# Optimization experiments

Measured on AMD Instinct MI355X. Metric: run time of the kernel, lower is better.

The kernel has to match this reference:

```python
import jax, jax.numpy as jnp
import numpy as np

SHAPES = ((64, 64), (32, 32), (16, 16))   # H/8, H/16, H/32 levels of a 512x512 image
B, D = 32, 256
NH, L, P = 8, 3, 4                        # MSDeformAttn heads / levels / points
DH = D // NH
NCLS, NC, NH_CA = 200, 10, 2
LQ = 32 * 32
LIN = sum(h * w for h, w in SHAPES)


def _ref_points():
    # get_reference_points for the H/16 grid, normalized (x, y) in (0,1)
    H_, W_ = 32, 32
    ry, rx = np.meshgrid(np.linspace(0.5, H_ - 0.5, H_) / H_,
                         np.linspace(0.5, W_ - 0.5, W_) / W_, indexing='ij')
    ref = np.stack([rx.ravel(), ry.ravel()], -1).astype(np.float32)  # (Lq, 2)
    return jnp.asarray(ref)[None, :, None, :]                        # (1, Lq, 1, 2)


def _msda(query, feats, W_off, b_off, W_attn, b_attn, W_val, b_val, W_out, b_out):
    """Multi-scale deformable attention (grid_sample bilinear, align_corners=False, zero pad)."""
    value = (feats @ W_val + b_val).reshape(B, LIN, NH, DH)
    off = (query @ W_off + b_off).reshape(B, LQ, NH, L, P, 2)
    aw = jax.nn.softmax((query @ W_attn + b_attn).reshape(B, LQ, NH, L * P), -1)
    aw = aw.reshape(B, LQ, NH, L, P)
    norm = jnp.asarray([[w, h] for h, w in SHAPES], jnp.float32)     # (L, 2) as (W, H)
    ref = _ref_points()                                              # (1, Lq, 1, 2)
    loc = ref[:, :, None, :, None, :] + off / norm[None, None, None, :, None, :]  # (B,Lq,NH,L,P,2)

    out = jnp.zeros((B, NH, LQ, DH), query.dtype)
    start = 0
    for lvl, (H_, W_) in enumerate(SHAPES):
        v = value[:, start:start + H_ * W_].transpose(0, 2, 1, 3)    # (B, NH, HW, DH)
        start += H_ * W_
        lx = loc[:, :, :, lvl, :, 0] * W_ - 0.5                      # (B, Lq, NH, P)
        ly = loc[:, :, :, lvl, :, 1] * H_ - 0.5
        x0 = jnp.floor(lx).astype(jnp.int32)
        y0 = jnp.floor(ly).astype(jnp.int32)
        dx = (lx - x0).transpose(0, 2, 1, 3)                         # (B, NH, Lq, P)
        dy = (ly - y0).transpose(0, 2, 1, 3)

        def gather(ix, iy):
            valid = (ix >= 0) & (ix < W_) & (iy >= 0) & (iy < H_)
            idx = (jnp.clip(iy, 0, H_ - 1) * W_ + jnp.clip(ix, 0, W_ - 1))
            idx = idx.transpose(0, 2, 1, 3).reshape(B, NH, LQ * P)
            g = jnp.take_along_axis(v, idx[..., None], axis=2).reshape(B, NH, LQ, P, DH)
            return g * valid.transpose(0, 2, 1, 3)[..., None]

        samp = (gather(x0,     y0)     * ((1 - dx) * (1 - dy))[..., None]
              + gather(x0 + 1, y0)     * (dx * (1 - dy))[..., None]
              + gather(x0,     y0 + 1) * ((1 - dx) * dy)[..., None]
              + gather(x0 + 1, y0 + 1) * (dx * dy)[..., None])       # (B,NH,Lq,P,DH)
        out = out + (samp * aw[:, :, :, lvl, :].transpose(0, 2, 1, 3)[..., None]).sum(3)
    out = out.transpose(0, 2, 1, 3).reshape(B, LQ, D)
    return out @ W_out + b_out


def _cross_attn(x, concepts, Wq, bq, Wkv, bkv, Wp, bp):
    Bx, N, _ = x.shape
    M = concepts.shape[1]
    dh = D // NH_CA
    q = (x @ Wq + bq).reshape(Bx, N, NH_CA, dh).transpose(0, 2, 1, 3)          # (B, h, N, dh)
    kv = (concepts @ Wkv + bkv).reshape(1, M, 2, NH_CA, dh).transpose(2, 0, 3, 1, 4)
    k, v = kv[0], kv[1]                                                        # (1, h, M, dh)
    attn = jax.nn.softmax(jnp.einsum('bhnd,ohmd->bhnm', q, k) * (dh ** -0.5), -1)
    o = jnp.einsum('bhnm,ohmd->bhnd', attn, v).transpose(0, 2, 1, 3).reshape(Bx, N, D)
    return o @ Wp + bp, attn


def _forward(query, feats, x_cls, W_off, b_off, W_attn, b_attn, W_val, b_val, W_out, b_out,
             unsup_concepts, concepts, spatial_concepts,
             Wq_c, bq_c, Wkv_c, bkv_c, Wp_c, bp_c,
             Wq_s, bq_s, Wkv_s, bkv_s, Wp_s, bp_s):
    # injector-style residual: query tokens refined by multi-scale deformable attention
    x = query + _msda(query, feats, W_off, b_off, W_attn, b_attn, W_val, b_val, W_out, b_out)
    # NB: original code reuses concept_tranformer for the unsup branch (faithful to source)
    out_u, attn_u = _cross_attn(x_cls, unsup_concepts, Wq_c, bq_c, Wkv_c, bkv_c, Wp_c, bp_c)
    out_n, attn_n = _cross_attn(x_cls, concepts,       Wq_c, bq_c, Wkv_c, bkv_c, Wp_c, bp_c)
    out_s, attn_s = _cross_attn(x,     spatial_concepts, Wq_s, bq_s, Wkv_s, bkv_s, Wp_s, bp_s)
    out = out_u[:, 0] + out_n[:, 0] + out_s.mean(1)                  # (B, num_classes)
    return out, attn_u.mean(1), attn_n.mean(1), attn_s.mean(1)


def setup_inputs() -> dict:
    key = jax.random.key(0)
    ks = jax.random.split(key, 20)
    s = 1.0 / np.sqrt(D)

    def n(i, shape, scale=1.0):
        return jax.random.normal(ks[i], shape, jnp.float32) * scale

    return dict(
        query=n(0, (B, LQ, D)), feats=n(1, (B, LIN, D)), x_cls=n(2, (B, 1, D)),
        W_off=n(3, (D, NH * L * P * 2), 0.01), b_off=n(4, (NH * L * P * 2,), 0.5),
        W_attn=n(5, (D, NH * L * P), 0.01), b_attn=jnp.zeros((NH * L * P,)),
        W_val=n(6, (D, D), s), b_val=jnp.zeros((D,)),
        W_out=n(7, (D, D), s), b_out=jnp.zeros((D,)),
        unsup_concepts=n(8, (1, NC, D), s), concepts=n(9, (1, NC, D), s),
        spatial_concepts=n(10, (1, NC, D), s),
        Wq_c=n(11, (D, D), s), bq_c=jnp.zeros((D,)),
        Wkv_c=n(12, (D, 2 * D), s), bkv_c=jnp.zeros((2 * D,)),
        Wp_c=n(13, (D, NCLS), s), bp_c=jnp.zeros((NCLS,)),
        Wq_s=n(14, (D, D), s), bq_s=jnp.zeros((D,)),
        Wkv_s=n(15, (D, 2 * D), s), bkv_s=jnp.zeros((2 * D,)),
        Wp_s=n(16, (D, NCLS), s), bp_s=jnp.zeros((NCLS,)),
    )


def reference(query, feats, x_cls, W_off, b_off, W_attn, b_attn, W_val, b_val, W_out, b_out,
              unsup_concepts, concepts, spatial_concepts,
              Wq_c, bq_c, Wkv_c, bkv_c, Wp_c, bp_c,
              Wq_s, bq_s, Wkv_s, bkv_s, Wp_s, bp_s):
    return _forward(query, feats, x_cls, W_off, b_off, W_attn, b_attn, W_val, b_val, W_out, b_out,
                    unsup_concepts, concepts, spatial_concepts,
                    Wq_c, bq_c, Wkv_c, bkv_c, Wp_c, bp_c,
                    Wq_s, bq_s, Wkv_s, bkv_s, Wp_s, bp_s)
```

## Files before the change

kernel.cpp:

```cpp
#include <hip/hip_runtime.h>
#include <hip/hip_bf16.h>


typedef __attribute__((ext_vector_type(8))) short s16x8;
typedef __attribute__((ext_vector_type(4))) float f32x4;

__device__ __forceinline__ void store_val(float* p, float v) { *p = v; }
__device__ __forceinline__ void store_val(__hip_bfloat16* p, float v) { *p = __float2bfloat16(v); }

__device__ __forceinline__ unsigned short f2bf(float x) {
  unsigned int u = __builtin_bit_cast(unsigned int, x);
  u += 0x7FFFu + ((u >> 16) & 1u);
  return (unsigned short)(u >> 16);
}
__device__ __forceinline__ float bf2f(unsigned short u) {
  return __builtin_bit_cast(float, (unsigned int)u << 16);
}
__device__ __forceinline__ float bflo(unsigned int u) {
  return __builtin_bit_cast(float, u << 16);
}
__device__ __forceinline__ float bfhi(unsigned int u) {
  return __builtin_bit_cast(float, u & 0xFFFF0000u);
}

__device__ __forceinline__ void gload16(const char* g, char* l) {
  __builtin_amdgcn_global_load_lds(
      (const __attribute__((address_space(1))) unsigned int*)g,
      (__attribute__((address_space(3))) unsigned int*)l, 16, 0, 0);
}

__global__ __launch_bounds__(256) void prep_all(
    const float* __restrict__ W_val, const float* __restrict__ W_off,
    const float* __restrict__ b_off, const float* __restrict__ W_attn,
    const float* __restrict__ b_attn, char* __restrict__ imgV,
    char* __restrict__ imgQ, float* __restrict__ bpack,
    const float* __restrict__ unsup, const float* __restrict__ conc,
    const float* __restrict__ spat, const float* __restrict__ Wkv_c,
    const float* __restrict__ bkv_c, const float* __restrict__ Wkv_s,
    const float* __restrict__ bkv_s, float* __restrict__ kv_u,
    float* __restrict__ kv_n, float* __restrict__ kv_s,
    const float* __restrict__ Wq_s, const float* __restrict__ bq_s,
    const float* __restrict__ W_out, const float* __restrict__ b_out,
    float* __restrict__ WLt, float* __restrict__ WL2t, float* __restrict__ cL)
{
  const int bi = blockIdx.x;
  const int tid = threadIdx.x;
  if (bi <= 576) {
    const int n = bi, k = tid;
    if (n == 576) {
      bpack[k] = (k < 192) ? b_off[k] : ((k < 288) ? b_attn[k - 192] : 0.f);
      if (k < 64) bpack[256 + k] = (k < 32) ? b_attn[64 + k] : 0.f;
      return;
    }
    const int ks = k >> 6;
    const int kb = (k & 63) * 2;
    if (n < 256) {
      const unsigned short v = f2bf(W_val[(size_t)k * 256 + n]);
      *(unsigned short*)(imgV + ks * 32768 + n * 128 + (kb ^ ((n & 7) << 4))) = v;
    } else {
      const int c = n - 256;
      float v = 0.f;
      if (c < 192) v = W_off[(size_t)k * 192 + c];
      else if (c < 288) v = W_attn[(size_t)k * 96 + (c - 192)];
      *(unsigned short*)(imgQ + ks * 40960 + c * 128 + (kb ^ ((c & 7) << 4))) = f2bf(v);
    }
    return;
  }
  if (bi <= 579) {
    const int j = bi - 577;
    const float* src = (j == 0) ? unsup : ((j == 1) ? conc : spat);
    const float* W   = (j < 2) ? Wkv_c : Wkv_s;
    const float* bb  = (j < 2) ? bkv_c : bkv_s;
    float* dst       = (j == 0) ? kv_u : ((j == 1) ? kv_n : kv_s);
    __shared__ float s[2560];
    for (int i = tid; i < 2560; i += 256) s[i] = src[i];
    __syncthreads();
    for (int o = tid; o < 5120; o += 256) {
      const int m = o >> 9, n = o & 511;
      float acc = bb[n];
      for (int k = 0; k < 256; ++k) acc += s[m * 256 + k] * W[(size_t)k * 512 + n];
      dst[o] = acc;
    }
    return;
  }
  {
    const int j = bi - 580;
    const int h = j / 10, m = j % 10;
    __shared__ float kk[128], wl[256], bred[256];
    if (tid < 128) {
      const int n = h * 128 + tid;
      float acc = bkv_s[n];
      for (int k = 0; k < 256; ++k) acc += spat[m * 256 + k] * Wkv_s[(size_t)k * 512 + n];
      kk[tid] = acc;
    }
    __syncthreads();
    float acc = 0.f;
    for (int e = 0; e < 128; ++e) acc += Wq_s[(size_t)tid * 256 + h * 128 + e] * kk[e];
    wl[tid] = acc;
    __syncthreads();
    float acc2 = 0.f;
    for (int t = 0; t < 256; ++t) acc2 += W_out[(size_t)tid * 256 + t] * wl[t];
    const float scale = 0.08838834764831845f;
    WLt[j * 256 + tid] = scale * acc;
    WL2t[j * 256 + tid] = scale * acc2;
    bred[tid] = b_out[tid] * wl[tid] + ((tid < 128) ? bq_s[h * 128 + tid] * kk[tid] : 0.f);
    __syncthreads();
    for (int s = 128; s > 0; s >>= 1) {
      if (tid < s) bred[tid] += bred[tid + s];
      __syncthreads();
    }
    if (tid == 0) cL[j] = scale * bred[0];
  }
}

template <typename OT, int NCOLS, int MINW, bool HM>
__global__ __launch_bounds__(512, MINW) void gemm_f32a(
    const float* __restrict__ A, const char* __restrict__ Bimg,
    const float* __restrict__ bias, OT* __restrict__ C)
{
  constexpr int NFR = NCOLS / 64;
  __shared__ char sAf[32768];
  __shared__ char sBb[NCOLS * 128];

  const int tid = threadIdx.x;
  const int lane = tid & 63;
  const int w = tid >> 6;
  const int wr = (w >> 2) * 64;
  const int wc = (w & 3) * (NCOLS / 4);
  const int l15 = lane & 15;
  const int lg = lane >> 4;
  const int m0 = blockIdx.x * 128;

  int asrc[4];
#pragma unroll
  for (int i = 0; i < 4; ++i) {
    const int slot = w * 256 + i * 64 + lane;
    const int row = slot >> 4;
    const int c = (slot & 15) ^ (row & 7);
    asrc[i] = row * 256 + c * 4;
  }
  const float* Abase = A + (size_t)m0 * 256;

  f32x4 acc[4][NFR] = {};

#pragma unroll
  for (int ks = 0; ks < 4; ++ks) {
    if (ks) __syncthreads();
    {
      char* la = sAf + w * 4096;
#pragma unroll
      for (int i = 0; i < 4; ++i)
        gload16((const char*)(Abase + ks * 64 + asrc[i]), la + i * 1024);
      const char* gb = Bimg + ks * (NCOLS * 128) + w * (NCOLS * 16) + lane * 16;
      char* lb = sBb + w * (NCOLS * 16);
#pragma unroll
      for (int i = 0; i < NFR; ++i)
        gload16(gb + i * 1024, lb + i * 1024);
    }
    __syncthreads();
#pragma unroll
    for (int kk = 0; kk < 2; ++kk) {
      const int c0 = kk * 8 + lg * 2;
      s16x8 af[4];
#pragma unroll
      for (int mf = 0; mf < 4; ++mf) {
        const int row = wr + mf * 16 + l15;
        const int sw = row & 7;
        const f32x4 lo = *reinterpret_cast<const f32x4*>(
            sAf + row * 256 + ((c0 ^ sw) * 16));
        const f32x4 hi = *reinterpret_cast<const f32x4*>(
            sAf + row * 256 + (((c0 + 1) ^ sw) * 16));
        uint4 u;
        u.x = (unsigned)f2bf(lo[0]) | ((unsigned)f2bf(lo[1]) << 16);
        u.y = (unsigned)f2bf(lo[2]) | ((unsigned)f2bf(lo[3]) << 16);
        u.z = (unsigned)f2bf(hi[0]) | ((unsigned)f2bf(hi[1]) << 16);
        u.w = (unsigned)f2bf(hi[2]) | ((unsigned)f2bf(hi[3]) << 16);
        af[mf] = __builtin_bit_cast(s16x8, u);
      }
      const int kb = kk * 64 + lg * 16;
      s16x8 bf[NFR];
#pragma unroll
      for (int nf = 0; nf < NFR; ++nf) {
        const int col = wc + nf * 16 + l15;
        bf[nf] = *reinterpret_cast<const s16x8*>(sBb + col * 128 + (kb ^ ((col & 7) << 4)));
      }
#pragma unroll
      for (int mf = 0; mf < 4; ++mf)
#pragma unroll
        for (int nf = 0; nf < NFR; ++nf)
          acc[mf][nf] = __builtin_amdgcn_mfma_f32_16x16x32_bf16(af[mf], bf[nf], acc[mf][nf], 0, 0, 0);
    }
  }

#pragma unroll
  for (int nf = 0; nf < NFR; ++nf) {
    const int col = wc + nf * 16 + l15;
    const float bb = bias[col];
#pragma unroll
    for (int mf = 0; mf < 4; ++mf) {
#pragma unroll
      for (int j = 0; j < 4; ++j) {
        const int row = m0 + wr + mf * 16 + lg * 4 + j;
        const float v = acc[mf][nf][j] + bb;
        if constexpr (HM) {
          const unsigned rb = (unsigned)row / 5376u;
          const unsigned rr = (unsigned)row - rb * 5376u;
          store_val(&C[(((size_t)rb * 8 + (col >> 5)) * 5376 + rr) * 32 + (col & 31)], v);
        } else {
          store_val(&C[(size_t)row * NCOLS + col], v);
        }
      }
    }
  }
}

__global__ __launch_bounds__(256) void msda_v4(
    const float* __restrict__ offlog, const __hip_bfloat16* __restrict__ value,
    __hip_bfloat16* __restrict__ msda_out)
{
  const int bq0 = blockIdx.x * 8;
  const int b = bq0 >> 10;
  const int tid = threadIdx.x;
  __shared__ float aw[768];
  __shared__ int4 sRow[768];
  __shared__ float4 sW[768];
  __shared__ __align__(16) char gbuf[4 * 3 * 4096];

  if (tid < 64) {
    const int qi = tid >> 3, h = tid & 7;
    const float* lp = &offlog[(size_t)(bq0 + qi) * 320 + 192 + h * 12];
    float e[12];
    float mx = -1e30f;
#pragma unroll
    for (int i = 0; i < 12; ++i) { e[i] = lp[i]; mx = fmaxf(mx, e[i]); }
    float s = 0.f;
#pragma unroll
    for (int i = 0; i < 12; ++i) { e[i] = expf(e[i] - mx); s += e[i]; }
    const float inv = 1.f / s;
#pragma unroll
    for (int i = 0; i < 12; ++i) aw[qi * 96 + h * 12 + i] = e[i] * inv;
  }
  __syncthreads();

#pragma unroll
  for (int k = 0; k < 3; ++k) {
    const int j = k * 256 + tid;
    const int qi = j / 96, cc = j - qi * 96;
    const int q = (bq0 + qi) & 1023;
    const int h = cc / 12, r = cc - h * 12, l = r >> 2, p_ = r & 3;
    const int WHl[3] = {64, 32, 16};
    const int St[3] = {0, 4096, 5120};
    const float2 o2 = *reinterpret_cast<const float2*>(
        &offlog[(size_t)(bq0 + qi) * 320 + h * 24 + l * 8 + p_ * 2]);
    const float refx = ((q & 31) + 0.5f) * (1.0f / 32.0f);
    const float refy = ((q >> 5) + 0.5f) * (1.0f / 32.0f);
    const int WH = WHl[l];
    const float fw = (float)WH;
    const float lx = (refx + o2.x / fw) * fw - 0.5f;
    const float ly = (refy + o2.y / fw) * fw - 0.5f;
    const float fx = floorf(lx), fy = floorf(ly);
    const int x0 = (int)fx, y0 = (int)fy;
    const float dx = lx - fx, dy = ly - fy;
    const float a = aw[j];
    int rows[4];
    float ws[4];
#pragma unroll
    for (int c = 0; c < 4; ++c) {
      const int ix = x0 + (c & 1), iy = y0 + (c >> 1);
      const float wb = ((c & 1) ? dx : 1.f - dx) * ((c >> 1) ? dy : 1.f - dy);
      const bool valid = (ix >= 0) && (ix < WH) && (iy >= 0) && (iy < WH);
      const int cx = min(max(ix, 0), WH - 1);
      const int cy = min(max(iy, 0), WH - 1);
      rows[c] = St[l] + cy * WH + cx;
      ws[c] = valid ? wb * a : 0.f;
    }
    sRow[j] = int4{rows[0], rows[1], rows[2], rows[3]};
    sW[j] = float4{ws[0], ws[1], ws[2], ws[3]};
  }
  __syncthreads();

  const int w = tid >> 6;
  const int lane = tid & 63;
  const int qi = tid >> 5;
  const int h = (tid >> 2) & 7;
  const int d4 = tid & 3;
  const unsigned short* vb = (const unsigned short*)value
      + ((size_t)b * 8 + h) * 5376 * 32 + d4 * 8;
  const int cbase = qi * 96 + h * 12;
  char* gb = gbuf + w * 12288;

#pragma unroll
  for (int s0 = 0; s0 < 2; ++s0) {
    const int4 rows = sRow[cbase + s0];
    const int ra[4] = {rows.x, rows.y, rows.z, rows.w};
#pragma unroll
    for (int c = 0; c < 4; ++c)
      gload16((const char*)(vb + (size_t)ra[c] * 32), gb + s0 * 4096 + c * 1024);
  }

  float acc[8] = {};
#pragma unroll
  for (int s = 0; s < 12; ++s) {
    if (s + 2 < 12) {
      const int4 rows = sRow[cbase + s + 2];
      const int ra[4] = {rows.x, rows.y, rows.z, rows.w};
      const int slot = (s + 2) % 3;
#pragma unroll
      for (int c = 0; c < 4; ++c)
        gload16((const char*)(vb + (size_t)ra[c] * 32), gb + slot * 4096 + c * 1024);
    }
    if (s <= 9)       asm volatile("s_waitcnt vmcnt(8)" ::: "memory");
    else if (s == 10) asm volatile("s_waitcnt vmcnt(4)" ::: "memory");
    else              asm volatile("s_waitcnt vmcnt(0)" ::: "memory");
    __builtin_amdgcn_sched_barrier(0);
    const float4 wv = sW[cbase + s];
    const float wa[4] = {wv.x, wv.y, wv.z, wv.w};
    const int slot = s % 3;
#pragma unroll
    for (int c = 0; c < 4; ++c) {
      const uint4 v = *reinterpret_cast<const uint4*>(gb + slot * 4096 + c * 1024 + lane * 16);
      const float wgt = wa[c];
      acc[0] += wgt * bflo(v.x); acc[1] += wgt * bfhi(v.x);
      acc[2] += wgt * bflo(v.y); acc[3] += wgt * bfhi(v.y);
      acc[4] += wgt * bflo(v.z); acc[5] += wgt * bfhi(v.z);
      acc[6] += wgt * bflo(v.w); acc[7] += wgt * bfhi(v.w);
    }
  }
  uint4 o;
  o.x = (unsigned)f2bf(acc[0]) | ((unsigned)f2bf(acc[1]) << 16);
  o.y = (unsigned)f2bf(acc[2]) | ((unsigned)f2bf(acc[3]) << 16);
  o.z = (unsigned)f2bf(acc[4]) | ((unsigned)f2bf(acc[5]) << 16);
  o.w = (unsigned)f2bf(acc[6]) | ((unsigned)f2bf(acc[7]) << 16);
  *reinterpret_cast<uint4*>(
      (unsigned short*)msda_out + (size_t)(bq0 + qi) * 256 + h * 32 + d4 * 8) = o;
}

__global__ __launch_bounds__(256) void spatial_kernel(
    const float* __restrict__ query, const __hip_bfloat16* __restrict__ msda,
    const float* __restrict__ WLt, const float* __restrict__ WL2t,
    const float* __restrict__ cL, float* __restrict__ attn_out,
    float* __restrict__ partial)
{
  __shared__ float wls[20][256];
  __shared__ float wl2s[20][256];
  __shared__ float red[128][20];
  const int tid = threadIdx.x;
  for (int i = tid; i < 5120; i += 256) {
    wls[i >> 8][i & 255] = WLt[i];
    wl2s[i >> 8][i & 255] = WL2t[i];
  }
  const int row_local = tid >> 1;
  const int half = tid & 1;
  const int row = blockIdx.x * 128 + row_local;
  float acc[20];
#pragma unroll
  for (int c = 0; c < 20; ++c) acc[c] = half ? 0.f : cL[c];
  __syncthreads();

  const float* qp = &query[(size_t)row * 256 + half * 128];
  const unsigned short* mp = (const unsigned short*)msda + (size_t)row * 256 + half * 128;
  const int kbase = half * 128;
  for (int k = 0; k < 128; k += 4) {
    const f32x4 q4 = *reinterpret_cast<const f32x4*>(qp + k);
    const uint2 mm = *reinterpret_cast<const uint2*>(mp + k);
    const float m0 = bf2f((unsigned short)mm.x);
    const float m1 = bf2f((unsigned short)(mm.x >> 16));
    const float m2 = bf2f((unsigned short)mm.y);
    const float m3 = bf2f((unsigned short)(mm.y >> 16));
#pragma unroll
    for (int c = 0; c < 20; ++c) {
      const f32x4 w4 = *reinterpret_cast<const f32x4*>(&wls[c][kbase + k]);
      const f32x4 v4 = *reinterpret_cast<const f32x4*>(&wl2s[c][kbase + k]);
      acc[c] += q4.x * w4.x + q4.y * w4.y + q4.z * w4.z + q4.w * w4.w
              + m0 * v4.x + m1 * v4.y + m2 * v4.z + m3 * v4.w;
    }
  }
  if (half == 1) {
#pragma unroll
    for (int c = 0; c < 20; ++c) red[row_local][c] = acc[c];
  }
  __syncthreads();
  if (half == 0) {
    float a[20];
#pragma unroll
    for (int c = 0; c < 20; ++c) a[c] = acc[c] + red[row_local][c];
#pragma unroll
    for (int h = 0; h < 2; ++h) {
      float mx = -1e30f;
#pragma unroll
      for (int m = 0; m < 10; ++m) mx = fmaxf(mx, a[h * 10 + m]);
      float s = 0.f;
#pragma unroll
      for (int m = 0; m < 10; ++m) { a[h * 10 + m] = expf(a[h * 10 + m] - mx); s += a[h * 10 + m]; }
      const float inv = 1.f / s;
#pragma unroll
      for (int m = 0; m < 10; ++m) a[h * 10 + m] *= inv;
    }
#pragma unroll
    for (int m = 0; m < 10; ++m)
      attn_out[(size_t)row * 10 + m] = 0.5f * (a[m] + a[10 + m]);
#pragma unroll
    for (int c = 0; c < 20; ++c) red[row_local][c] = a[c];
  }
  __syncthreads();
  if (tid < 20) {
    float s = 0.f;
    for (int r = 0; r < 128; ++r) s += red[r][tid];
    partial[blockIdx.x * 20 + tid] = s;
  }
}

__global__ __launch_bounds__(256) void final2_kernel(
    const float* __restrict__ x_cls, const float* __restrict__ Wq_c,
    const float* __restrict__ bq_c, const float* __restrict__ kv_u,
    const float* __restrict__ kv_n, const float* __restrict__ partial,
    const float* __restrict__ kv_s, const float* __restrict__ Wp_c,
    const float* __restrict__ bp_c, const float* __restrict__ Wp_s,
    const float* __restrict__ bp_s, float* __restrict__ out,
    float* __restrict__ attn_u_out, float* __restrict__ attn_n_out)
{
  const int b = blockIdx.x, tid = threadIdx.x;
  __shared__ float ou[256], osb[256], abar[20], xr[256];
  if (tid < 64)
    *reinterpret_cast<float4*>(&xr[tid * 4]) =
        *reinterpret_cast<const float4*>(&x_cls[(size_t)b * 256 + tid * 4]);
  if (tid >= 64 && tid < 84) {
    const int c = tid - 64;
    float s = 0.f;
    for (int ch = 0; ch < 8; ++ch) s += partial[(b * 8 + ch) * 20 + c];
    abar[c] = s * (1.0f / 1024.0f);
  }
  __syncthreads();
  if (tid < 64) {
    const int lane = tid;
    float4 q4 = *reinterpret_cast<const float4*>(&bq_c[lane * 4]);
    for (int k = 0; k < 256; ++k) {
      const float xk = xr[k];
      const float4 w = *reinterpret_cast<const float4*>(&Wq_c[(size_t)k * 256 + lane * 4]);
      q4.x += xk * w.x; q4.y += xk * w.y; q4.z += xk * w.z; q4.w += xk * w.w;
    }
    const float scale = 0.08838834764831845f;
    float4 osum = {0.f, 0.f, 0.f, 0.f};
    for (int cs = 0; cs < 2; ++cs) {
      const float* kv = cs ? kv_n : kv_u;
      float* aout = cs ? attn_n_out : attn_u_out;
      float attn[10];
      float mx = -1e30f;
#pragma unroll
      for (int m = 0; m < 10; ++m) {
        const float4 k4 = *reinterpret_cast<const float4*>(&kv[m * 512 + lane * 4]);
        float p = q4.x * k4.x + q4.y * k4.y + q4.z * k4.z + q4.w * k4.w;
        p += __shfl_xor(p, 1);  p += __shfl_xor(p, 2);  p += __shfl_xor(p, 4);
        p += __shfl_xor(p, 8);  p += __shfl_xor(p, 16);
        attn[m] = p * scale;
        mx = fmaxf(mx, attn[m]);
      }
      float s = 0.f;
#pragma unroll
      for (int m = 0; m < 10; ++m) { attn[m] = expf(attn[m] - mx); s += attn[m]; }
      const float inv = 1.f / s;
#pragma unroll
      for (int m = 0; m < 10; ++m) {
        attn[m] *= inv;
        const float am = 0.5f * (attn[m] + __shfl_xor(attn[m], 32));
        if (lane == m) aout[b * 10 + m] = am;
        const float4 v4 = *reinterpret_cast<const float4*>(&kv[m * 512 + 256 + lane * 4]);
        osum.x += attn[m] * v4.x; osum.y += attn[m] * v4.y;
        osum.z += attn[m] * v4.z; osum.w += attn[m] * v4.w;
      }
    }
    *reinterpret_cast<float4*>(&ou[lane * 4]) = osum;
  }
  {
    const int h = tid >> 7, d = tid & 127;
    float s = 0.f;
#pragma unroll
    for (int m = 0; m < 10; ++m) s += abar[h * 10 + m] * kv_s[m * 512 + 256 + h * 128 + d];
    osb[tid] = s;
  }
  __syncthreads();
  if (tid < 200) {
    float acc = 2.f * bp_c[tid] + bp_s[tid];
    for (int dd = 0; dd < 256; ++dd)
      acc += ou[dd] * Wp_c[dd * 200 + tid] + osb[dd] * Wp_s[dd * 200 + tid];
    out[b * 200 + tid] = acc;
  }
}

extern "C" void kernel_launch(void* const* d_in, const int* in_sizes, int n_in,
                              void* d_out, int out_size, void* d_ws, size_t ws_size,
                              hipStream_t stream)
{
  const float* query  = (const float*)d_in[0];
  const float* feats  = (const float*)d_in[1];
  const float* x_cls  = (const float*)d_in[2];
  const float* W_off  = (const float*)d_in[3];
  const float* b_off  = (const float*)d_in[4];
  const float* W_attn = (const float*)d_in[5];
  const float* b_attn = (const float*)d_in[6];
  const float* W_val  = (const float*)d_in[7];
  const float* b_val  = (const float*)d_in[8];
  const float* W_out  = (const float*)d_in[9];
  const float* b_out  = (const float*)d_in[10];
  const float* unsup  = (const float*)d_in[11];
  const float* conc   = (const float*)d_in[12];
  const float* spat   = (const float*)d_in[13];
  const float* Wq_c   = (const float*)d_in[14];
  const float* bq_c   = (const float*)d_in[15];
  const float* Wkv_c  = (const float*)d_in[16];
  const float* bkv_c  = (const float*)d_in[17];
  const float* Wp_c   = (const float*)d_in[18];
  const float* bp_c   = (const float*)d_in[19];
  const float* Wq_s   = (const float*)d_in[20];
  const float* bq_s   = (const float*)d_in[21];
  const float* Wkv_s  = (const float*)d_in[22];
  const float* bkv_s  = (const float*)d_in[23];
  const float* Wp_s   = (const float*)d_in[24];
  const float* bp_s   = (const float*)d_in[25];
  float* out = (float*)d_out;

  const int B = 32, LQ = 1024, LIN = 5376;
  const int MQ = B * LQ;
  const int MV = B * LIN;

  char* p = (char*)d_ws;
  __hip_bfloat16* value = (__hip_bfloat16*)p;   p += (size_t)MV * 256 * 2;
  float* offlog   = (float*)p;                  p += (size_t)MQ * 320 * 4;
  __hip_bfloat16* msda = (__hip_bfloat16*)p;    p += (size_t)MQ * 256 * 2;
  char* imgV      = p;                          p += 4 * 32768;
  char* imgQ      = p;                          p += 4 * 40960;
  float* bpack    = (float*)p;                  p += 320 * 4;
  float* kv_u     = (float*)p;                  p += 5120 * 4;
  float* kv_n     = (float*)p;                  p += 5120 * 4;
  float* kv_s     = (float*)p;                  p += 5120 * 4;
  float* WLt      = (float*)p;                  p += 5120 * 4;
  float* WL2t     = (float*)p;                  p += 5120 * 4;
  float* cL       = (float*)p;                  p += 32 * 4;
  float* partial  = (float*)p;                  p += 256 * 20 * 4;

  dim3 blk(256);
  prep_all<<<dim3(600), blk, 0, stream>>>(
      W_val, W_off, b_off, W_attn, b_attn, imgV, imgQ, bpack,
      unsup, conc, spat, Wkv_c, bkv_c, Wkv_s, bkv_s, kv_u, kv_n, kv_s,
      Wq_s, bq_s, W_out, b_out, WLt, WL2t, cL);
  gemm_f32a<__hip_bfloat16, 256, 4, true><<<dim3(MV / 128), dim3(512), 0, stream>>>(
      feats, imgV, b_val, value);
  gemm_f32a<float, 320, 2, false><<<dim3(MQ / 128), dim3(512), 0, stream>>>(
      query, imgQ, bpack, offlog);
  msda_v4<<<dim3(MQ / 8), blk, 0, stream>>>(offlog, value, msda);
  spatial_kernel<<<dim3(MQ / 128), blk, 0, stream>>>(
      query, msda, WLt, WL2t, cL, out + 7040, partial);
  final2_kernel<<<dim3(B), blk, 0, stream>>>(
      x_cls, Wq_c, bq_c, kv_u, kv_n, partial, kv_s, Wp_c, bp_c, Wp_s, bp_s,
      out, out + 6400, out + 6720);
}
```

Baseline: 317.5 us.

## Fuse spatial concept-attention logits into MSDA kernel epilogue

Merges the spatial_kernel into the deformable attention kernel: each thread dots its fp32 MSDA accumulator slice and query slice against the fused weight rows, then reduces across 32 lanes with shuffles before computing the softmax. This removes the bf16 MSDA intermediate buffer's write and read and one kernel launch. In exchange, every thread in the MSDA kernel reads 20x2 weight rows from global memory (cached) and performs 100 shuffles, and the partial-sum array grows 16x, so final2 must sum 128 chunks per batch.

```diff
diff --git a/kernel.cpp b/kernel.cpp
--- a/kernel.cpp
+++ b/kernel.cpp
@@ -214,9 +214,11 @@
   }
 }
 
-__global__ __launch_bounds__(256) void msda_v4(
+__global__ __launch_bounds__(256) void msda_sp(
     const float* __restrict__ offlog, const __hip_bfloat16* __restrict__ value,
-    __hip_bfloat16* __restrict__ msda_out)
+    const float* __restrict__ query, const float* __restrict__ WLt,
+    const float* __restrict__ WL2t, const float* __restrict__ cL,
+    float* __restrict__ attn_out, float* __restrict__ partial)
 {
   const int bq0 = blockIdx.x * 8;
   const int b = bq0 >> 10;
@@ -225,6 +227,7 @@
   __shared__ int4 sRow[768];
   __shared__ float4 sW[768];
   __shared__ __align__(16) char gbuf[4 * 3 * 4096];
+  __shared__ float ared[8][20];
 
   if (tid < 64) {
     const int qi = tid >> 3, h = tid & 7;
@@ -326,86 +329,58 @@
       acc[6] += wgt * bflo(v.w); acc[7] += wgt * bfhi(v.w);
     }
   }
-  uint4 o;
-  o.x = (unsigned)f2bf(acc[0]) | ((unsigned)f2bf(acc[1]) << 16);
-  o.y = (unsigned)f2bf(acc[2]) | ((unsigned)f2bf(acc[3]) << 16);
-  o.z = (unsigned)f2bf(acc[4]) | ((unsigned)f2bf(acc[5]) << 16);
-  o.w = (unsigned)f2bf(acc[6]) | ((unsigned)f2bf(acc[7]) << 16);
-  *reinterpret_cast<uint4*>(
-      (unsigned short*)msda_out + (size_t)(bq0 + qi) * 256 + h * 32 + d4 * 8) = o;
-}
-
-__global__ __launch_bounds__(256) void spatial_kernel(
-    const float* __restrict__ query, const __hip_bfloat16* __restrict__ msda,
-    const float* __restrict__ WLt, const float* __restrict__ WL2t,
-    const float* __restrict__ cL, float* __restrict__ attn_out,
-    float* __restrict__ partial)
-{
-  __shared__ float wls[20][256];
-  __shared__ float wl2s[20][256];
-  __shared__ float red[128][20];
-  const int tid = threadIdx.x;
-  for (int i = tid; i < 5120; i += 256) {
-    wls[i >> 8][i & 255] = WLt[i];
-    wl2s[i >> 8][i & 255] = WL2t[i];
-  }
-  const int row_local = tid >> 1;
-  const int half = tid & 1;
-  const int row = blockIdx.x * 128 + row_local;
-  float acc[20];
-#pragma unroll
-  for (int c = 0; c < 20; ++c) acc[c] = half ? 0.f : cL[c];
-  __syncthreads();
-
-  const float* qp = &query[(size_t)row * 256 + half * 128];
-  const unsigned short* mp = (const unsigned short*)msda + (size_t)row * 256 + half * 128;
-  const int kbase = half * 128;
-  for (int k = 0; k < 128; k += 4) {
-    const f32x4 q4 = *reinterpret_cast<const f32x4*>(qp + k);
-    const uint2 mm = *reinterpret_cast<const uint2*>(mp + k);
-    const float m0 = bf2f((unsigned short)mm.x);
-    const float m1 = bf2f((unsigned short)(mm.x >> 16));
-    const float m2 = bf2f((unsigned short)mm.y);
-    const float m3 = bf2f((unsigned short)(mm.y >> 16));
-#pragma unroll
-    for (int c = 0; c < 20; ++c) {
-      const f32x4 w4 = *reinterpret_cast<const f32x4*>(&wls[c][kbase + k]);
-      const f32x4 v4 = *reinterpret_cast<const f32x4*>(&wl2s[c][kbase + k]);
-      acc[c] += q4.x * w4.x + q4.y * w4.y + q4.z * w4.z + q4.w * w4.w
-              + m0 * v4.x + m1 * v4.y + m2 * v4.z + m3 * v4.w;
-    }
-  }
-  if (half == 1) {
-#pragma unroll
-    for (int c = 0; c < 20; ++c) red[row_local][c] = acc[c];
-  }
-  __syncthreads();
-  if (half == 0) {
+
+  const int kq = (tid & 31) * 8;
+  const float* qp = &query[(size_t)(bq0 + qi) * 256 + kq];
+  const f32x4 q0 = *reinterpret_cast<const f32x4*>(qp);
+  const f32x4 q1 = *reinterpret_cast<const f32x4*>(qp + 4);
+  float lg2[20];
+#pragma unroll
+  for (int c = 0; c < 20; ++c) {
+    const f32x4 w0 = *reinterpret_cast<const f32x4*>(&WLt[c * 256 + kq]);
+    const f32x4 w1 = *reinterpret_cast<const f32x4*>(&WLt[c * 256 + kq + 4]);
+    const f32x4 v0 = *reinterpret_cast<const f32x4*>(&WL2t[c * 256 + kq]);
+    const f32x4 v1 = *reinterpret_cast<const f32x4*>(&WL2t[c * 256 + kq + 4]);
+    lg2[c] = q0.x * w0.x + q0.y * w0.y + q0.z * w0.z + q0.w * w0.w
+           + q1.x * w1.x + q1.y * w1.y + q1.z * w1.z + q1.w * w1.w
+           + acc[0] * v0.x + acc[1] * v0.y + acc[2] * v0.z + acc[3] * v0.w
+           + acc[4] * v1.x + acc[5] * v1.y + acc[6] * v1.z + acc[7] * v1.w;
+  }
+#pragma unroll
+  for (int c = 0; c < 20; ++c) {
+    lg2[c] += __shfl_xor(lg2[c], 1);
+    lg2[c] += __shfl_xor(lg2[c], 2);
+    lg2[c] += __shfl_xor(lg2[c], 4);
+    lg2[c] += __shfl_xor(lg2[c], 8);
+    lg2[c] += __shfl_xor(lg2[c], 16);
+  }
+  if ((tid & 31) == 0) {
     float a[20];
 #pragma unroll
-    for (int c = 0; c < 20; ++c) a[c] = acc[c] + red[row_local][c];
-#pragma unroll
-    for (int h = 0; h < 2; ++h) {
+    for (int c = 0; c < 20; ++c) a[c] = lg2[c] + cL[c];
+#pragma unroll
+    for (int hh = 0; hh < 2; ++hh) {
       float mx = -1e30f;
 #pragma unroll
-      for (int m = 0; m < 10; ++m) mx = fmaxf(mx, a[h * 10 + m]);
+      for (int m = 0; m < 10; ++m) mx = fmaxf(mx, a[hh * 10 + m]);
       float s = 0.f;
 #pragma unroll
-      for (int m = 0; m < 10; ++m) { a[h * 10 + m] = expf(a[h * 10 + m] - mx); s += a[h * 10 + m]; }
+      for (int m = 0; m < 10; ++m) { a[hh * 10 + m] = expf(a[hh * 10 + m] - mx); s += a[hh * 10 + m]; }
       const float inv = 1.f / s;
 #pragma unroll
-      for (int m = 0; m < 10; ++m) a[h * 10 + m] *= inv;
+      for (int m = 0; m < 10; ++m) a[hh * 10 + m] *= inv;
     }
 #pragma unroll
     for (int m = 0; m < 10; ++m)
-      attn_out[(size_t)row * 10 + m] = 0.5f * (a[m] + a[10 + m]);
-#pragma unroll
-    for (int c = 0; c < 20; ++c) red[row_local][c] = a[c];
+      attn_out[(size_t)(bq0 + qi) * 10 + m] = 0.5f * (a[m] + a[10 + m]);
+#pragma unroll
+    for (int c = 0; c < 20; ++c) ared[qi][c] = a[c];
   }
   __syncthreads();
   if (tid < 20) {
     float s = 0.f;
-    for (int r = 0; r < 128; ++r) s += red[r][tid];
+#pragma unroll
+    for (int q2 = 0; q2 < 8; ++q2) s += ared[q2][tid];
     partial[blockIdx.x * 20 + tid] = s;
   }
 }
@@ -427,7 +402,7 @@
   if (tid >= 64 && tid < 84) {
     const int c = tid - 64;
     float s = 0.f;
-    for (int ch = 0; ch < 8; ++ch) s += partial[(b * 8 + ch) * 20 + c];
+    for (int ch = 0; ch < 128; ++ch) s += partial[((size_t)b * 128 + ch) * 20 + c];
     abar[c] = s * (1.0f / 1024.0f);
   }
   __syncthreads();
@@ -526,7 +501,6 @@
   char* p = (char*)d_ws;
   __hip_bfloat16* value = (__hip_bfloat16*)p;   p += (size_t)MV * 256 * 2;
   float* offlog   = (float*)p;                  p += (size_t)MQ * 320 * 4;
-  __hip_bfloat16* msda = (__hip_bfloat16*)p;    p += (size_t)MQ * 256 * 2;
   char* imgV      = p;                          p += 4 * 32768;
   char* imgQ      = p;                          p += 4 * 40960;
   float* bpack    = (float*)p;                  p += 320 * 4;
@@ -536,7 +510,7 @@
   float* WLt      = (float*)p;                  p += 5120 * 4;
   float* WL2t     = (float*)p;                  p += 5120 * 4;
   float* cL       = (float*)p;                  p += 32 * 4;
-  float* partial  = (float*)p;                  p += 256 * 20 * 4;
+  float* partial  = (float*)p;                  p += 4096 * 20 * 4;
 
   dim3 blk(256);
   prep_all<<<dim3(600), blk, 0, stream>>>(
@@ -547,9 +521,8 @@
       feats, imgV, b_val, value);
   gemm_f32a<float, 320, 2, false><<<dim3(MQ / 128), dim3(512), 0, stream>>>(
       query, imgQ, bpack, offlog);
-  msda_v4<<<dim3(MQ / 8), blk, 0, stream>>>(offlog, value, msda);
-  spatial_kernel<<<dim3(MQ / 128), blk, 0, stream>>>(
-      query, msda, WLt, WL2t, cL, out + 7040, partial);
+  msda_sp<<<dim3(MQ / 8), blk, 0, stream>>>(
+      offlog, value, query, WLt, WL2t, cL, out + 7040, partial);
   final2_kernel<<<dim3(B), blk, 0, stream>>>(
       x_cls, Wq_c, bq_c, kv_u, kv_n, partial, kv_s, Wp_c, bp_c, Wp_s, bp_s,
       out, out + 6400, out + 6720);
```

After: 331.5 us. 4.4% more time.
